# Optimization experiments

Measured on AMD Instinct MI355X. Metric: run time of the kernel, lower is better.

## Reference

```python
import jax, jax.numpy as jnp
import numpy as np

VOCAB, P, K, B, L, R = 50257, 512, 64, 32, 2048, 5


def setup_inputs() -> dict:
    key = jax.random.key(0)
    k1, k2, k3, k4, k5, k6, k7 = jax.random.split(key, 7)
    return {
        "x": jax.random.randint(k1, (B, L), 0, VOCAB, dtype=jnp.int32),
        "V": jax.random.normal(k2, (VOCAB, P), dtype=jnp.float32),
        "C": jax.random.normal(k3, (K, P), dtype=jnp.float32),
        "f1_w": jax.random.normal(k4, (2 * R + 1,), dtype=jnp.float32),
        "f1_b": jax.random.normal(k5, (K,), dtype=jnp.float32),
        "f2_w": jax.random.normal(k6, (K, P), dtype=jnp.float32),
        "f2_b": jax.random.normal(k7, (K,), dtype=jnp.float32),
    }


def reference(x, V, C, f1_w, f1_b, f2_w, f2_b):
    b, l = x.shape
    k, p = C.shape
    w = f1_w.shape[0]
    r = (w - 1) // 2
    emb = V[x]                                              # [B,L,P] embedding lookup
    x_hat = emb / jnp.linalg.norm(emb, axis=2, keepdims=True)
    l_hat = C / jnp.linalg.norm(C, axis=1, keepdims=True)
    G = jnp.einsum('kp,blp->bkl', l_hat, x_hat)             # cosine sim [B,K,L]
    # sliding-window dot product == depthwise 1D cross-correlation, 'same' padding
    u = jax.lax.conv_general_dilated(
        G.reshape(b * k, 1, l), f1_w.reshape(1, 1, w),
        window_strides=(1,), padding=[(r, r)],
        dimension_numbers=('NCH', 'OIH', 'NCH'),
    ).reshape(b, k, l)
    m = jax.nn.relu(u + f1_b[None, :, None])                # [B,K,L]
    beta = jax.nn.softmax(m.max(axis=1), axis=1)            # max over labels, softmax over seq -> [B,L]
    pooled = jnp.mean(beta[:, :, None] * emb, axis=1)       # [B,P]
    return pooled @ f2_w.T + f2_b                           # [B,K]
```

## Files before the change

### kernel.cpp

```cpp
#include <hip/hip_runtime.h>
#include <hip/hip_bf16.h>

#define PP     512
#define KK     64
#define BB     32
#define LLEN   2048
#define NPOS   (BB * LLEN)

typedef __attribute__((ext_vector_type(8)))  short short8;
typedef __attribute__((ext_vector_type(16))) float float16;

__device__ inline unsigned int pack_bf2(float lo, float hi) {
    __hip_bfloat162 h = __float22bfloat162_rn(make_float2(lo, hi));
    unsigned int u;
    __builtin_memcpy(&u, &h, 4);
    return u;
}
__device__ inline float bf_lo(unsigned int v) { return __uint_as_float(v << 16); }
__device__ inline float bf_hi(unsigned int v) { return __uint_as_float(v & 0xffff0000u); }

__global__ void k1_prep(const float* __restrict__ C, const float* __restrict__ f2w,
                        ushort* __restrict__ Bu) {
    const int n = blockIdx.x;
    const float* src = (n < 64) ? (C + n * PP) : (f2w + (n - 64) * PP);
    const int t = threadIdx.x;
    float v0 = src[t];
    float v1 = src[t + 256];
    __shared__ float red[256];
    red[t] = v0 * v0 + v1 * v1;
    __syncthreads();
    for (int s = 128; s > 0; s >>= 1) {
        if (t < s) red[t] += red[t + s];
        __syncthreads();
    }
    const float inv = (n < 64) ? rsqrtf(red[0]) : 1.f;
    Bu[(((t >> 3)       * 128 + n) << 3) + (t & 7)] = (ushort)(pack_bf2(v0 * inv, 0.f) & 0xffffu);
    Bu[((((t + 256) >> 3)) * 128 + n) * 8 + (t & 7)] = (ushort)(pack_bf2(v1 * inv, 0.f) & 0xffffu);
}

__launch_bounds__(256)
__global__ void k2_gemm(const int* __restrict__ x, const float* __restrict__ V,
                        const uint4* __restrict__ Bu4,
                        unsigned int* __restrict__ Gt2, unsigned int* __restrict__ E2p) {
    __shared__ uint4 sA[64 * 64];
    __shared__ int   stok[64];
    __shared__ float rnorm[64];

    const int tid  = threadIdx.x;
    const int lane = tid & 63;
    const int wv   = tid >> 6;
    const int r    = tid >> 2;
    const int q    = tid & 3;

    if (tid < 64) stok[tid] = x[blockIdx.x * 64 + tid];
    __syncthreads();

    const float* src = V + (size_t)stok[r] * PP + q * 4;
    const int swzr = r & 7;
    float nrm = 0.f;

    float4 pa[16];
#pragma unroll
    for (int g = 0; g < 16; ++g) pa[g] = ((const float4*)src)[g * 4];
    float4 pb[16];
#pragma unroll
    for (int g = 0; g < 16; ++g) pb[g] = ((const float4*)src)[(g + 16) * 4];

#pragma unroll
    for (int g = 0; g < 16; ++g) {
        const float4 a = pa[g];
        nrm = fmaf(a.x, a.x, fmaf(a.y, a.y, fmaf(a.z, a.z, fmaf(a.w, a.w, nrm))));
        uint2 w2; w2.x = pack_bf2(a.x, a.y); w2.y = pack_bf2(a.z, a.w);
        const int f = g * 2 + (q >> 1);
        ((uint2*)&sA[r * 64 + (f ^ swzr)])[q & 1] = w2;
    }
#pragma unroll
    for (int g = 0; g < 16; ++g) {
        const float4 a = pb[g];
        nrm = fmaf(a.x, a.x, fmaf(a.y, a.y, fmaf(a.z, a.z, fmaf(a.w, a.w, nrm))));
        uint2 w2; w2.x = pack_bf2(a.x, a.y); w2.y = pack_bf2(a.z, a.w);
        const int f = (g + 16) * 2 + (q >> 1);
        ((uint2*)&sA[r * 64 + (f ^ swzr)])[q & 1] = w2;
    }

    nrm += __shfl_xor(nrm, 1, 64);
    nrm += __shfl_xor(nrm, 2, 64);
    if (q == 0) rnorm[r] = rsqrtf(nrm);
    __syncthreads();

    float16 acc0, acc1;
#pragma unroll
    for (int i = 0; i < 16; ++i) { acc0[i] = 0.f; acc1[i] = 0.f; }

    const int mt  = (wv & 1) * 32;
    const int nh  = (wv >> 1) * 64;
    const int l31 = lane & 31;
    const int cc  = lane >> 5;
    const int mq  = mt + l31;
    const int abase = mq * 64;
    const int aswz  = mq & 7;

#pragma unroll 8
    for (int ks = 0; ks < 32; ++ks) {
        const int ff = ks * 2 + cc;
        const uint4 av = sA[abase + (ff ^ aswz)];
        const uint4 b0 = Bu4[ff * 128 + nh + l31];
        const uint4 b1 = Bu4[ff * 128 + nh + 32 + l31];
        short8 a8, t0, t1;
        __builtin_memcpy(&a8, &av, 16);
        __builtin_memcpy(&t0, &b0, 16);
        __builtin_memcpy(&t1, &b1, 16);
        acc0 = __builtin_amdgcn_mfma_f32_32x32x16_bf16(a8, t0, acc0, 0, 0, 0);
        acc1 = __builtin_amdgcn_mfma_f32_32x32x16_bf16(a8, t1, acc1, 0, 0, 0);
    }

    const size_t posBase = (size_t)blockIdx.x * 64;
#pragma unroll
    for (int reg = 0; reg < 16; ++reg) {
        const int rr = (reg & 3) + 8 * (reg >> 2) + 4 * (lane >> 5);
        const int m  = mt + rr;
        const size_t p = posBase + m;
        if (wv < 2) {
            const float rn = rnorm[m];
            Gt2[p * 32 + l31] = pack_bf2(acc0[reg] * rn, acc1[reg] * rn);
        } else {
            E2p[p * 32 + l31] = pack_bf2(acc0[reg], acc1[reg]);
        }
    }
}

__global__ void k3_convpool(const unsigned int* __restrict__ Gt2,
                            const unsigned int* __restrict__ E2p,
                            const float* __restrict__ f1w, const float* __restrict__ f1b,
                            float* __restrict__ pool) {
    __shared__ unsigned int sT[74 * 33];
    __shared__ float smv[64];
    __shared__ float sp[64];
    __shared__ float sscal[2];
    __shared__ float sred[8][64];

    const int b  = blockIdx.x >> 5;
    const int l0 = (blockIdx.x & 31) * 64;
    const int t  = threadIdx.x;

    for (int idx = t; idx < 74 * 32; idx += 256) {
        const int row = idx >> 5, col = idx & 31;
        const int gl = l0 - 5 + row;
        sT[row * 33 + col] = (gl >= 0 && gl < LLEN)
            ? Gt2[((size_t)b * LLEN + gl) * 32 + col] : 0u;
    }
    __syncthreads();

    float w[11];
#pragma unroll
    for (int j = 0; j < 11; ++j) w[j] = f1w[j];
    const int j = t & 31;
    const int h = t >> 5;
    const float bias0 = f1b[j], bias1 = f1b[j + 32];
#pragma unroll
    for (int i = 0; i < 8; ++i) {
        const int lr = i * 8 + h;
        float u0 = 0.f, u1 = 0.f;
#pragma unroll
        for (int tap = 0; tap < 11; ++tap) {
            const unsigned int v = sT[(lr + tap) * 33 + j];
            u0 = fmaf(bf_lo(v), w[tap], u0);
            u1 = fmaf(bf_hi(v), w[tap], u1);
        }
        float m = fmaxf(fmaxf(u0 + bias0, 0.f), fmaxf(u1 + bias1, 0.f));
#pragma unroll
        for (int off = 16; off > 0; off >>= 1)
            m = fmaxf(m, __shfl_xor(m, off, 64));
        if (j == 0) smv[lr] = m;
    }
    __syncthreads();

    if (t < 64) {
        float v = smv[t];
#pragma unroll
        for (int off = 32; off > 0; off >>= 1)
            v = fmaxf(v, __shfl_xor(v, off, 64));
        if (t == 0) sscal[0] = v;
    }
    __syncthreads();
    const float mx = sscal[0];
    if (t < 64) sp[t] = __expf(smv[t] - mx);
    __syncthreads();
    if (t < 64) {
        float s = sp[t];
#pragma unroll
        for (int off = 32; off > 0; off >>= 1)
            s += __shfl_xor(s, off, 64);
        if (t == 0) sscal[1] = s;
    }

    float a0 = 0.f, a1 = 0.f;
#pragma unroll
    for (int i = 0; i < 8; ++i) {
        const int l = i * 8 + h;
        const float wgt = sp[l];
        const unsigned int e = E2p[((size_t)b * LLEN + l0 + l) * 32 + j];
        a0 = fmaf(wgt, bf_lo(e), a0);
        a1 = fmaf(wgt, bf_hi(e), a1);
    }
    sred[h][j]      = a0;
    sred[h][j + 32] = a1;
    __syncthreads();
    if (t < 64) {
        float r = 0.f;
#pragma unroll
        for (int hh = 0; hh < 8; ++hh) r += sred[hh][t];
        float* dst = pool + (size_t)blockIdx.x * 68;
        dst[t] = r;
        if (t == 0) { dst[64] = sscal[0]; dst[65] = sscal[1]; }
    }
}

__global__ void k6_final(const float* __restrict__ pool, const float* __restrict__ f2b,
                         float* __restrict__ out) {
    const int b = blockIdx.x;
    const int k = threadIdx.x;
    float M = -1e30f;
#pragma unroll
    for (int c = 0; c < 32; ++c)
        M = fmaxf(M, pool[(size_t)(b * 32 + c) * 68 + 64]);
    float tot = 0.f, num = 0.f;
#pragma unroll
    for (int c = 0; c < 32; ++c) {
        const float* pc = pool + (size_t)(b * 32 + c) * 68;
        const float sc = __expf(pc[64] - M);
        tot = fmaf(sc, pc[65], tot);
        num = fmaf(sc, pc[k], num);
    }
    out[b * KK + k] = (num / tot) * (1.f / 2048.f) + f2b[k];
}

extern "C" void kernel_launch(void* const* d_in, const int* in_sizes, int n_in,
                              void* d_out, int out_size, void* d_ws, size_t ws_size,
                              hipStream_t stream) {
    const int*   x   = (const int*)d_in[0];
    const float* V   = (const float*)d_in[1];
    const float* C   = (const float*)d_in[2];
    const float* f1w = (const float*)d_in[3];
    const float* f1b = (const float*)d_in[4];
    const float* f2w = (const float*)d_in[5];
    const float* f2b = (const float*)d_in[6];
    float* out = (float*)d_out;

    float* ws = (float*)d_ws;
    ushort* Bu = (ushort*)ws;
    unsigned int* Gt2 = (unsigned int*)(ws + 32768);
    unsigned int* E2p = Gt2 + (size_t)NPOS * 32;
    float* pool = (float*)(E2p + (size_t)NPOS * 32);

    k1_prep    <<<128, 256, 0, stream>>>(C, f2w, Bu);
    k2_gemm    <<<NPOS / 64, 256, 0, stream>>>(x, V, (const uint4*)Bu, Gt2, E2p);
    k3_convpool<<<BB * 32, 256, 0, stream>>>(Gt2, E2p, f1w, f1b, pool);
    k6_final   <<<BB, 64, 0, stream>>>(pool, f2b, out);
}
```

Baseline: 190.3 us.

## Warp-specialize GEMM into producer/consumer waves with double-buffered LDS tiles

The embedding GEMM kernel now splits its four waves into two producer waves that gather, normalize and pack 32-token tiles into a double-buffered LDS area, and two consumer waves that run the MFMA loop on the previous tile. Each block processes four tiles, so the gather latency of the next tile overlaps the matrix math of the current one. Rows are pre-normalized before the bf16 packing, and the norm is stored separately and reapplied in the pooling kernel so the E projection stays unnormalized. In exchange, half the waves do no MFMA work, there are half as many blocks, and an extra norm array is read in the conv/pool kernel.

```diff
diff --git a/kernel.cpp b/kernel.cpp
--- a/kernel.cpp
+++ b/kernel.cpp
@@ -41,96 +41,129 @@
 __launch_bounds__(256)
 __global__ void k2_gemm(const int* __restrict__ x, const float* __restrict__ V,
                         const uint4* __restrict__ Bu4,
-                        unsigned int* __restrict__ Gt2, unsigned int* __restrict__ E2p) {
-    __shared__ uint4 sA[64 * 64];
-    __shared__ int   stok[64];
-    __shared__ float rnorm[64];
+                        unsigned int* __restrict__ Gt2, unsigned int* __restrict__ E2p,
+                        float* __restrict__ vnorm) {
+    __shared__ uint4 sA[2][32 * 64];
 
     const int tid  = threadIdx.x;
     const int lane = tid & 63;
     const int wv   = tid >> 6;
-    const int r    = tid >> 2;
-    const int q    = tid & 3;
-
-    if (tid < 64) stok[tid] = x[blockIdx.x * 64 + tid];
-    __syncthreads();
-
-    const float* src = V + (size_t)stok[r] * PP + q * 4;
-    const int swzr = r & 7;
-    float nrm = 0.f;
-
-    float4 pa[16];
-#pragma unroll
-    for (int g = 0; g < 16; ++g) pa[g] = ((const float4*)src)[g * 4];
-    float4 pb[16];
-#pragma unroll
-    for (int g = 0; g < 16; ++g) pb[g] = ((const float4*)src)[(g + 16) * 4];
-
-#pragma unroll
-    for (int g = 0; g < 16; ++g) {
-        const float4 a = pa[g];
-        nrm = fmaf(a.x, a.x, fmaf(a.y, a.y, fmaf(a.z, a.z, fmaf(a.w, a.w, nrm))));
-        uint2 w2; w2.x = pack_bf2(a.x, a.y); w2.y = pack_bf2(a.z, a.w);
-        const int f = g * 2 + (q >> 1);
-        ((uint2*)&sA[r * 64 + (f ^ swzr)])[q & 1] = w2;
-    }
-#pragma unroll
-    for (int g = 0; g < 16; ++g) {
-        const float4 a = pb[g];
-        nrm = fmaf(a.x, a.x, fmaf(a.y, a.y, fmaf(a.z, a.z, fmaf(a.w, a.w, nrm))));
-        uint2 w2; w2.x = pack_bf2(a.x, a.y); w2.y = pack_bf2(a.z, a.w);
-        const int f = (g + 16) * 2 + (q >> 1);
-        ((uint2*)&sA[r * 64 + (f ^ swzr)])[q & 1] = w2;
-    }
-
-    nrm += __shfl_xor(nrm, 1, 64);
-    nrm += __shfl_xor(nrm, 2, 64);
-    if (q == 0) rnorm[r] = rsqrtf(nrm);
-    __syncthreads();
-
-    float16 acc0, acc1;
-#pragma unroll
-    for (int i = 0; i < 16; ++i) { acc0[i] = 0.f; acc1[i] = 0.f; }
-
-    const int mt  = (wv & 1) * 32;
-    const int nh  = (wv >> 1) * 64;
+    const bool producer = (wv >= 2);
+    const int tile0 = blockIdx.x * 4;
+
+    const int pidx = tid & 127;
+    const int pr   = pidx >> 2;
+    const int pq   = pidx & 3;
+
+    if (producer) {
+        const int tok = x[tile0 * 32 + pr];
+        const float* src = V + (size_t)tok * PP + pq * 4;
+        float4 pa[16], pb[16];
+#pragma unroll
+        for (int g = 0; g < 16; ++g) pa[g] = ((const float4*)src)[g * 4];
+#pragma unroll
+        for (int g = 0; g < 16; ++g) pb[g] = ((const float4*)src)[(g + 16) * 4];
+        float nrm = 0.f;
+#pragma unroll
+        for (int g = 0; g < 16; ++g) {
+            const float4 a = pa[g], b = pb[g];
+            nrm = fmaf(a.x, a.x, fmaf(a.y, a.y, fmaf(a.z, a.z, fmaf(a.w, a.w, nrm))));
+            nrm = fmaf(b.x, b.x, fmaf(b.y, b.y, fmaf(b.z, b.z, fmaf(b.w, b.w, nrm))));
+        }
+        nrm += __shfl_xor(nrm, 1, 64);
+        nrm += __shfl_xor(nrm, 2, 64);
+        const float inv = rsqrtf(nrm);
+        if (pq == 0) vnorm[tile0 * 32 + pr] = sqrtf(nrm);
+        const int swz = pr & 7;
+#pragma unroll
+        for (int g = 0; g < 16; ++g) {
+            const float4 a = pa[g];
+            uint2 w2; w2.x = pack_bf2(a.x * inv, a.y * inv); w2.y = pack_bf2(a.z * inv, a.w * inv);
+            ((uint2*)&sA[0][pr * 64 + ((2 * g + (pq >> 1)) ^ swz)])[pq & 1] = w2;
+        }
+#pragma unroll
+        for (int g = 0; g < 16; ++g) {
+            const float4 a = pb[g];
+            uint2 w2; w2.x = pack_bf2(a.x * inv, a.y * inv); w2.y = pack_bf2(a.z * inv, a.w * inv);
+            ((uint2*)&sA[0][pr * 64 + ((2 * (g + 16) + (pq >> 1)) ^ swz)])[pq & 1] = w2;
+        }
+    }
+    __syncthreads();
+
     const int l31 = lane & 31;
     const int cc  = lane >> 5;
-    const int mq  = mt + l31;
-    const int abase = mq * 64;
-    const int aswz  = mq & 7;
-
+    const int nh  = (wv & 1) * 64;
+    const int abase = l31 * 64;
+    const int aswz  = l31 & 7;
+
+    for (int t = 0; t < 4; ++t) {
+        const int buf = t & 1;
+        if (!producer) {
+            float16 acc0, acc1;
+#pragma unroll
+            for (int i = 0; i < 16; ++i) { acc0[i] = 0.f; acc1[i] = 0.f; }
 #pragma unroll 8
-    for (int ks = 0; ks < 32; ++ks) {
-        const int ff = ks * 2 + cc;
-        const uint4 av = sA[abase + (ff ^ aswz)];
-        const uint4 b0 = Bu4[ff * 128 + nh + l31];
-        const uint4 b1 = Bu4[ff * 128 + nh + 32 + l31];
-        short8 a8, t0, t1;
-        __builtin_memcpy(&a8, &av, 16);
-        __builtin_memcpy(&t0, &b0, 16);
-        __builtin_memcpy(&t1, &b1, 16);
-        acc0 = __builtin_amdgcn_mfma_f32_32x32x16_bf16(a8, t0, acc0, 0, 0, 0);
-        acc1 = __builtin_amdgcn_mfma_f32_32x32x16_bf16(a8, t1, acc1, 0, 0, 0);
-    }
-
-    const size_t posBase = (size_t)blockIdx.x * 64;
-#pragma unroll
-    for (int reg = 0; reg < 16; ++reg) {
-        const int rr = (reg & 3) + 8 * (reg >> 2) + 4 * (lane >> 5);
-        const int m  = mt + rr;
-        const size_t p = posBase + m;
-        if (wv < 2) {
-            const float rn = rnorm[m];
-            Gt2[p * 32 + l31] = pack_bf2(acc0[reg] * rn, acc1[reg] * rn);
-        } else {
-            E2p[p * 32 + l31] = pack_bf2(acc0[reg], acc1[reg]);
-        }
+            for (int ks = 0; ks < 32; ++ks) {
+                const int ff = ks * 2 + cc;
+                const uint4 av = sA[buf][abase + (ff ^ aswz)];
+                const uint4 b0 = Bu4[ff * 128 + nh + l31];
+                const uint4 b1 = Bu4[ff * 128 + nh + 32 + l31];
+                short8 a8, t0, t1;
+                __builtin_memcpy(&a8, &av, 16);
+                __builtin_memcpy(&t0, &b0, 16);
+                __builtin_memcpy(&t1, &b1, 16);
+                acc0 = __builtin_amdgcn_mfma_f32_32x32x16_bf16(a8, t0, acc0, 0, 0, 0);
+                acc1 = __builtin_amdgcn_mfma_f32_32x32x16_bf16(a8, t1, acc1, 0, 0, 0);
+            }
+            const size_t posBase = (size_t)(tile0 + t) * 32;
+            unsigned int* dst = (wv == 0) ? Gt2 : E2p;
+#pragma unroll
+            for (int reg = 0; reg < 16; ++reg) {
+                const int rr = (reg & 3) + 8 * (reg >> 2) + 4 * cc;
+                dst[(posBase + rr) * 32 + l31] = pack_bf2(acc0[reg], acc1[reg]);
+            }
+        } else if (t < 3) {
+            const int tile = tile0 + t + 1;
+            const int tok = x[tile * 32 + pr];
+            const float* src = V + (size_t)tok * PP + pq * 4;
+            float4 pa[16], pb[16];
+#pragma unroll
+            for (int g = 0; g < 16; ++g) pa[g] = ((const float4*)src)[g * 4];
+#pragma unroll
+            for (int g = 0; g < 16; ++g) pb[g] = ((const float4*)src)[(g + 16) * 4];
+            float nrm = 0.f;
+#pragma unroll
+            for (int g = 0; g < 16; ++g) {
+                const float4 a = pa[g], b = pb[g];
+                nrm = fmaf(a.x, a.x, fmaf(a.y, a.y, fmaf(a.z, a.z, fmaf(a.w, a.w, nrm))));
+                nrm = fmaf(b.x, b.x, fmaf(b.y, b.y, fmaf(b.z, b.z, fmaf(b.w, b.w, nrm))));
+            }
+            nrm += __shfl_xor(nrm, 1, 64);
+            nrm += __shfl_xor(nrm, 2, 64);
+            const float inv = rsqrtf(nrm);
+            if (pq == 0) vnorm[tile * 32 + pr] = sqrtf(nrm);
+            const int swz = pr & 7;
+            const int bb = buf ^ 1;
+#pragma unroll
+            for (int g = 0; g < 16; ++g) {
+                const float4 a = pa[g];
+                uint2 w2; w2.x = pack_bf2(a.x * inv, a.y * inv); w2.y = pack_bf2(a.z * inv, a.w * inv);
+                ((uint2*)&sA[bb][pr * 64 + ((2 * g + (pq >> 1)) ^ swz)])[pq & 1] = w2;
+            }
+#pragma unroll
+            for (int g = 0; g < 16; ++g) {
+                const float4 a = pb[g];
+                uint2 w2; w2.x = pack_bf2(a.x * inv, a.y * inv); w2.y = pack_bf2(a.z * inv, a.w * inv);
+                ((uint2*)&sA[bb][pr * 64 + ((2 * (g + 16) + (pq >> 1)) ^ swz)])[pq & 1] = w2;
+            }
+        }
+        __syncthreads();
     }
 }
 
 __global__ void k3_convpool(const unsigned int* __restrict__ Gt2,
                             const unsigned int* __restrict__ E2p,
+                            const float* __restrict__ vnorm,
                             const float* __restrict__ f1w, const float* __restrict__ f1b,
                             float* __restrict__ pool) {
     __shared__ unsigned int sT[74 * 33];
@@ -198,7 +231,7 @@
 #pragma unroll
     for (int i = 0; i < 8; ++i) {
         const int l = i * 8 + h;
-        const float wgt = sp[l];
+        const float wgt = sp[l] * vnorm[b * LLEN + l0 + l];
         const unsigned int e = E2p[((size_t)b * LLEN + l0 + l) * 32 + j];
         a0 = fmaf(wgt, bf_lo(e), a0);
         a1 = fmaf(wgt, bf_hi(e), a1);
@@ -251,10 +284,11 @@
     ushort* Bu = (ushort*)ws;
     unsigned int* Gt2 = (unsigned int*)(ws + 32768);
     unsigned int* E2p = Gt2 + (size_t)NPOS * 32;
-    float* pool = (float*)(E2p + (size_t)NPOS * 32);
+    float* pool  = (float*)(E2p + (size_t)NPOS * 32);
+    float* vnorm = pool + 1024 * 68;
 
     k1_prep    <<<128, 256, 0, stream>>>(C, f2w, Bu);
-    k2_gemm    <<<NPOS / 64, 256, 0, stream>>>(x, V, (const uint4*)Bu, Gt2, E2p);
-    k3_convpool<<<BB * 32, 256, 0, stream>>>(Gt2, E2p, f1w, f1b, pool);
+    k2_gemm    <<<NPOS / 128, 256, 0, stream>>>(x, V, (const uint4*)Bu, Gt2, E2p, vnorm);
+    k3_convpool<<<BB * 32, 256, 0, stream>>>(Gt2, E2p, vnorm, f1w, f1b, pool);
     k6_final   <<<BB, 64, 0, stream>>>(pool, f2b, out);
 }
```

New measurement: 195.5 us. 2.7% more time.

## Fuse embedding GEMM with conv/softmax pooling, recomputing halo rows in-block

Applied to the files above, without the earlier changes.

Merges the embedding-gather GEMM and the conv/pooling kernel into one kernel. Each block now computes 80 rows (64 positions plus an 8-row halo on each side) with 16x16x32 MFMAs, and the P dimension is split into two halves so the loads of the second half overlap the MMAs of the first. G and E stay in shared memory, which removes the global write and re-read of the intermediate G and E tensors. In exchange, the halo rows are gathered and multiplied redundantly, and the larger shared-memory footprint may lower occupancy.

```diff
diff --git a/kernel.cpp b/kernel.cpp
--- a/kernel.cpp
+++ b/kernel.cpp
@@ -7,8 +7,8 @@
 #define LLEN   2048
 #define NPOS   (BB * LLEN)
 
-typedef __attribute__((ext_vector_type(8)))  short short8;
-typedef __attribute__((ext_vector_type(16))) float float16;
+typedef __attribute__((ext_vector_type(8))) short short8;
+typedef __attribute__((ext_vector_type(4))) float floatx4;
 
 __device__ inline unsigned int pack_bf2(float lo, float hi) {
     __hip_bfloat162 h = __float22bfloat162_rn(make_float2(lo, hi));
@@ -18,6 +18,7 @@
 }
 __device__ inline float bf_lo(unsigned int v) { return __uint_as_float(v << 16); }
 __device__ inline float bf_hi(unsigned int v) { return __uint_as_float(v & 0xffff0000u); }
+__device__ inline ushort bf16u(float v) { return (ushort)(pack_bf2(v, 0.f) & 0xffffu); }
 
 __global__ void k1_prep(const float* __restrict__ C, const float* __restrict__ f2w,
                         ushort* __restrict__ Bu) {
@@ -34,120 +35,172 @@
         __syncthreads();
     }
     const float inv = (n < 64) ? rsqrtf(red[0]) : 1.f;
-    Bu[(((t >> 3)       * 128 + n) << 3) + (t & 7)] = (ushort)(pack_bf2(v0 * inv, 0.f) & 0xffffu);
-    Bu[((((t + 256) >> 3)) * 128 + n) * 8 + (t & 7)] = (ushort)(pack_bf2(v1 * inv, 0.f) & 0xffffu);
+    Bu[(((t >> 3)        * 128 + n) << 3) + (t & 7)] = bf16u(v0 * inv);
+    Bu[((((t + 256) >> 3)) * 128 + n) * 8 + (t & 7)] = bf16u(v1 * inv);
 }
 
 __launch_bounds__(256)
-__global__ void k2_gemm(const int* __restrict__ x, const float* __restrict__ V,
+__global__ void k2_mega(const int* __restrict__ x, const float* __restrict__ V,
                         const uint4* __restrict__ Bu4,
-                        unsigned int* __restrict__ Gt2, unsigned int* __restrict__ E2p) {
-    __shared__ uint4 sA[64 * 64];
-    __shared__ int   stok[64];
-    __shared__ float rnorm[64];
-
-    const int tid  = threadIdx.x;
-    const int lane = tid & 63;
-    const int wv   = tid >> 6;
-    const int r    = tid >> 2;
-    const int q    = tid & 3;
-
-    if (tid < 64) stok[tid] = x[blockIdx.x * 64 + tid];
-    __syncthreads();
-
-    const float* src = V + (size_t)stok[r] * PP + q * 4;
-    const int swzr = r & 7;
-    float nrm = 0.f;
-
-    float4 pa[16];
-#pragma unroll
-    for (int g = 0; g < 16; ++g) pa[g] = ((const float4*)src)[g * 4];
-    float4 pb[16];
-#pragma unroll
-    for (int g = 0; g < 16; ++g) pb[g] = ((const float4*)src)[(g + 16) * 4];
-
-#pragma unroll
-    for (int g = 0; g < 16; ++g) {
-        const float4 a = pa[g];
-        nrm = fmaf(a.x, a.x, fmaf(a.y, a.y, fmaf(a.z, a.z, fmaf(a.w, a.w, nrm))));
-        uint2 w2; w2.x = pack_bf2(a.x, a.y); w2.y = pack_bf2(a.z, a.w);
-        const int f = g * 2 + (q >> 1);
-        ((uint2*)&sA[r * 64 + (f ^ swzr)])[q & 1] = w2;
-    }
-#pragma unroll
-    for (int g = 0; g < 16; ++g) {
-        const float4 a = pb[g];
-        nrm = fmaf(a.x, a.x, fmaf(a.y, a.y, fmaf(a.z, a.z, fmaf(a.w, a.w, nrm))));
-        uint2 w2; w2.x = pack_bf2(a.x, a.y); w2.y = pack_bf2(a.z, a.w);
-        const int f = (g + 16) * 2 + (q >> 1);
-        ((uint2*)&sA[r * 64 + (f ^ swzr)])[q & 1] = w2;
-    }
-
-    nrm += __shfl_xor(nrm, 1, 64);
-    nrm += __shfl_xor(nrm, 2, 64);
-    if (q == 0) rnorm[r] = rsqrtf(nrm);
-    __syncthreads();
-
-    float16 acc0, acc1;
-#pragma unroll
-    for (int i = 0; i < 16; ++i) { acc0[i] = 0.f; acc1[i] = 0.f; }
-
-    const int mt  = (wv & 1) * 32;
-    const int nh  = (wv >> 1) * 64;
-    const int l31 = lane & 31;
-    const int cc  = lane >> 5;
-    const int mq  = mt + l31;
-    const int abase = mq * 64;
-    const int aswz  = mq & 7;
-
-#pragma unroll 8
-    for (int ks = 0; ks < 32; ++ks) {
-        const int ff = ks * 2 + cc;
-        const uint4 av = sA[abase + (ff ^ aswz)];
-        const uint4 b0 = Bu4[ff * 128 + nh + l31];
-        const uint4 b1 = Bu4[ff * 128 + nh + 32 + l31];
-        short8 a8, t0, t1;
-        __builtin_memcpy(&a8, &av, 16);
-        __builtin_memcpy(&t0, &b0, 16);
-        __builtin_memcpy(&t1, &b1, 16);
-        acc0 = __builtin_amdgcn_mfma_f32_32x32x16_bf16(a8, t0, acc0, 0, 0, 0);
-        acc1 = __builtin_amdgcn_mfma_f32_32x32x16_bf16(a8, t1, acc1, 0, 0, 0);
-    }
-
-    const size_t posBase = (size_t)blockIdx.x * 64;
-#pragma unroll
-    for (int reg = 0; reg < 16; ++reg) {
-        const int rr = (reg & 3) + 8 * (reg >> 2) + 4 * (lane >> 5);
-        const int m  = mt + rr;
-        const size_t p = posBase + m;
-        if (wv < 2) {
-            const float rn = rnorm[m];
-            Gt2[p * 32 + l31] = pack_bf2(acc0[reg] * rn, acc1[reg] * rn);
-        } else {
-            E2p[p * 32 + l31] = pack_bf2(acc0[reg], acc1[reg]);
-        }
-    }
-}
-
-__global__ void k3_convpool(const unsigned int* __restrict__ Gt2,
-                            const unsigned int* __restrict__ E2p,
-                            const float* __restrict__ f1w, const float* __restrict__ f1b,
-                            float* __restrict__ pool) {
-    __shared__ unsigned int sT[74 * 33];
+                        const float* __restrict__ f1w, const float* __restrict__ f1b,
+                        float* __restrict__ pool) {
+    __shared__ uint4 sA[80 * 32];
+    __shared__ int   stok[80];
+    __shared__ float rnorm[80];
     __shared__ float smv[64];
     __shared__ float sp[64];
     __shared__ float sscal[2];
     __shared__ float sred[8][64];
 
-    const int b  = blockIdx.x >> 5;
-    const int l0 = (blockIdx.x & 31) * 64;
-    const int t  = threadIdx.x;
-
-    for (int idx = t; idx < 74 * 32; idx += 256) {
-        const int row = idx >> 5, col = idx & 31;
-        const int gl = l0 - 5 + row;
-        sT[row * 33 + col] = (gl >= 0 && gl < LLEN)
-            ? Gt2[((size_t)b * LLEN + gl) * 32 + col] : 0u;
+    const int t   = threadIdx.x;
+    const int b   = blockIdx.x >> 5;
+    const int l0  = (blockIdx.x & 31) * 64;
+
+    if (t < 80) {
+        int l = l0 - 8 + t;
+        l = l < 0 ? 0 : (l >= LLEN ? LLEN - 1 : l);
+        stok[t] = x[b * LLEN + l];
+    }
+    __syncthreads();
+
+    const int pr = t >> 2,  pq = t & 3;
+    const int sr = 64 + (t >> 4), sq = t & 15;
+    const float4* prow = (const float4*)(V + (size_t)stok[pr] * PP);
+    const float4* srow = (const float4*)(V + (size_t)stok[sr] * PP);
+
+    float4 p1[16];
+#pragma unroll
+    for (int g = 0; g < 16; ++g) p1[g] = prow[pq * 16 + g];
+    float4 s1[4];
+#pragma unroll
+    for (int g = 0; g < 4; ++g) s1[g] = srow[sq * 4 + g];
+
+    float np = 0.f, ns = 0.f;
+    const int pswz = pr & 7, sswz = sr & 7;
+#pragma unroll
+    for (int g = 0; g < 16; ++g) {
+        const float4 a = p1[g];
+        np = fmaf(a.x, a.x, fmaf(a.y, a.y, fmaf(a.z, a.z, fmaf(a.w, a.w, np))));
+        uint2 w2; w2.x = pack_bf2(a.x, a.y); w2.y = pack_bf2(a.z, a.w);
+        const int f = pq * 8 + (g >> 1);
+        ((uint2*)&sA[pr * 32 + (f ^ pswz)])[g & 1] = w2;
+    }
+#pragma unroll
+    for (int g = 0; g < 4; ++g) {
+        const float4 a = s1[g];
+        ns = fmaf(a.x, a.x, fmaf(a.y, a.y, fmaf(a.z, a.z, fmaf(a.w, a.w, ns))));
+        uint2 w2; w2.x = pack_bf2(a.x, a.y); w2.y = pack_bf2(a.z, a.w);
+        const int f = sq * 2 + (g >> 1);
+        ((uint2*)&sA[sr * 32 + (f ^ sswz)])[g & 1] = w2;
+    }
+
+    float4 p2[16];
+#pragma unroll
+    for (int g = 0; g < 16; ++g) p2[g] = prow[64 + pq * 16 + g];
+    float4 s2[4];
+#pragma unroll
+    for (int g = 0; g < 4; ++g) s2[g] = srow[64 + sq * 4 + g];
+
+    __syncthreads();
+
+    const int lane = t & 63, wv = t >> 6;
+    const int c15  = lane & 15;
+    const int quad = lane >> 4;
+    const int aswz = c15 & 7;
+    const int n0   = (wv * 2) * 16 + c15;
+    const int n1   = (wv * 2 + 1) * 16 + c15;
+
+    floatx4 acc[5][2];
+#pragma unroll
+    for (int m = 0; m < 5; ++m) {
+        acc[m][0] = (floatx4){0.f, 0.f, 0.f, 0.f};
+        acc[m][1] = (floatx4){0.f, 0.f, 0.f, 0.f};
+    }
+
+#pragma unroll
+    for (int ks = 0; ks < 8; ++ks) {
+        const int fl = ks * 4 + quad;
+        const uint4 b0 = Bu4[fl * 128 + n0];
+        const uint4 b1 = Bu4[fl * 128 + n1];
+        short8 bb0, bb1;
+        __builtin_memcpy(&bb0, &b0, 16);
+        __builtin_memcpy(&bb1, &b1, 16);
+#pragma unroll
+        for (int m = 0; m < 5; ++m) {
+            const uint4 av = sA[(m * 16 + c15) * 32 + (fl ^ aswz)];
+            short8 a8; __builtin_memcpy(&a8, &av, 16);
+            acc[m][0] = __builtin_amdgcn_mfma_f32_16x16x32_bf16(a8, bb0, acc[m][0], 0, 0, 0);
+            acc[m][1] = __builtin_amdgcn_mfma_f32_16x16x32_bf16(a8, bb1, acc[m][1], 0, 0, 0);
+        }
+    }
+    __syncthreads();
+
+#pragma unroll
+    for (int g = 0; g < 16; ++g) {
+        const float4 a = p2[g];
+        np = fmaf(a.x, a.x, fmaf(a.y, a.y, fmaf(a.z, a.z, fmaf(a.w, a.w, np))));
+        uint2 w2; w2.x = pack_bf2(a.x, a.y); w2.y = pack_bf2(a.z, a.w);
+        const int f = pq * 8 + (g >> 1);
+        ((uint2*)&sA[pr * 32 + (f ^ pswz)])[g & 1] = w2;
+    }
+#pragma unroll
+    for (int g = 0; g < 4; ++g) {
+        const float4 a = s2[g];
+        ns = fmaf(a.x, a.x, fmaf(a.y, a.y, fmaf(a.z, a.z, fmaf(a.w, a.w, ns))));
+        uint2 w2; w2.x = pack_bf2(a.x, a.y); w2.y = pack_bf2(a.z, a.w);
+        const int f = sq * 2 + (g >> 1);
+        ((uint2*)&sA[sr * 32 + (f ^ sswz)])[g & 1] = w2;
+    }
+    np += __shfl_xor(np, 1, 64);
+    np += __shfl_xor(np, 2, 64);
+    if (pq == 0) rnorm[pr] = rsqrtf(np);
+    ns += __shfl_xor(ns, 1, 64);
+    ns += __shfl_xor(ns, 2, 64);
+    ns += __shfl_xor(ns, 4, 64);
+    ns += __shfl_xor(ns, 8, 64);
+    if (sq == 0) rnorm[sr] = rsqrtf(ns);
+    __syncthreads();
+
+#pragma unroll
+    for (int ks = 0; ks < 8; ++ks) {
+        const int fl = ks * 4 + quad;
+        const uint4 b0 = Bu4[(32 + fl) * 128 + n0];
+        const uint4 b1 = Bu4[(32 + fl) * 128 + n1];
+        short8 bb0, bb1;
+        __builtin_memcpy(&bb0, &b0, 16);
+        __builtin_memcpy(&bb1, &b1, 16);
+#pragma unroll
+        for (int m = 0; m < 5; ++m) {
+            const uint4 av = sA[(m * 16 + c15) * 32 + (fl ^ aswz)];
+            short8 a8; __builtin_memcpy(&a8, &av, 16);
+            acc[m][0] = __builtin_amdgcn_mfma_f32_16x16x32_bf16(a8, bb0, acc[m][0], 0, 0, 0);
+            acc[m][1] = __builtin_amdgcn_mfma_f32_16x16x32_bf16(a8, bb1, acc[m][1], 0, 0, 0);
+        }
+    }
+    __syncthreads();
+
+    ushort* sG  = (ushort*)sA;
+    ushort* sE2 = (ushort*)sA + 80 * 66;
+    const bool isG = (wv < 2);
+#pragma unroll
+    for (int m = 0; m < 5; ++m) {
+#pragma unroll
+        for (int i = 0; i < 2; ++i) {
+            const int ccol = ((wv * 2 + i) * 16 + c15) & 63;
+            const int slot = (ccol & 31) * 2 + (ccol >> 5);
+#pragma unroll
+            for (int reg = 0; reg < 4; ++reg) {
+                const int row = m * 16 + quad * 4 + reg;
+                float v = acc[m][i][reg];
+                if (isG) {
+                    const int l = l0 - 8 + row;
+                    v = (l >= 0 && l < LLEN) ? v * rnorm[row] : 0.f;
+                    sG[row * 66 + slot] = bf16u(v);
+                } else {
+                    sE2[row * 66 + slot] = bf16u(v);
+                }
+            }
+        }
     }
     __syncthreads();
 
@@ -157,13 +210,14 @@
     const int j = t & 31;
     const int h = t >> 5;
     const float bias0 = f1b[j], bias1 = f1b[j + 32];
+    const uint* uG = (const uint*)sG;
 #pragma unroll
     for (int i = 0; i < 8; ++i) {
         const int lr = i * 8 + h;
         float u0 = 0.f, u1 = 0.f;
 #pragma unroll
         for (int tap = 0; tap < 11; ++tap) {
-            const unsigned int v = sT[(lr + tap) * 33 + j];
+            const unsigned int v = uG[(lr + 3 + tap) * 33 + j];
             u0 = fmaf(bf_lo(v), w[tap], u0);
             u1 = fmaf(bf_hi(v), w[tap], u1);
         }
@@ -194,12 +248,13 @@
         if (t == 0) sscal[1] = s;
     }
 
+    const uint* uE2 = (const uint*)sE2;
     float a0 = 0.f, a1 = 0.f;
 #pragma unroll
     for (int i = 0; i < 8; ++i) {
         const int l = i * 8 + h;
         const float wgt = sp[l];
-        const unsigned int e = E2p[((size_t)b * LLEN + l0 + l) * 32 + j];
+        const unsigned int e = uE2[(l + 8) * 33 + j];
         a0 = fmaf(wgt, bf_lo(e), a0);
         a1 = fmaf(wgt, bf_hi(e), a1);
     }
@@ -248,13 +303,10 @@
     float* out = (float*)d_out;
 
     float* ws = (float*)d_ws;
-    ushort* Bu = (ushort*)ws;
-    unsigned int* Gt2 = (unsigned int*)(ws + 32768);
-    unsigned int* E2p = Gt2 + (size_t)NPOS * 32;
-    float* pool = (float*)(E2p + (size_t)NPOS * 32);
-
-    k1_prep    <<<128, 256, 0, stream>>>(C, f2w, Bu);
-    k2_gemm    <<<NPOS / 64, 256, 0, stream>>>(x, V, (const uint4*)Bu, Gt2, E2p);
-    k3_convpool<<<BB * 32, 256, 0, stream>>>(Gt2, E2p, f1w, f1b, pool);
-    k6_final   <<<BB, 64, 0, stream>>>(pool, f2b, out);
-}
+    ushort* Bu  = (ushort*)ws;
+    float* pool = ws + 32768;
+
+    k1_prep<<<128, 256, 0, stream>>>(C, f2w, Bu);
+    k2_mega<<<BB * 32, 256, 0, stream>>>(x, V, (const uint4*)Bu, f1w, f1b, pool);
+    k6_final<<<BB, 64, 0, stream>>>(pool, f2b, out);
+}
```

After: 196.0 us. 1.03x slower.
